# Performance work log

Measured on AMD Instinct MI355X. Metric: run time of the kernel, lower is better.

Reference implementation:

```python
import jax, jax.numpy as jnp
import numpy as np

N = 64
EPS = 1e-4
N_ITER = 100
BRANCH = 10


def setup_inputs() -> dict:
    key = jax.random.key(0)
    x = jax.random.normal(key, (8192, 4096), dtype=jnp.float32)
    return {"x": x}


def _lml(x):
    # x: [n_batch, nx], nx > N assumed (as configured in setup_inputs)
    n_batch, nx = x.shape
    x_sorted = jnp.sort(x, axis=1)[:, ::-1]  # descending
    nu_lower = -x_sorted[:, N - 1] - 7.0  # [n_batch]
    nu_upper = -x_sorted[:, N] + 7.0      # [n_batch]
    ls = jnp.linspace(0.0, 1.0, BRANCH).astype(x.dtype)  # [branch]
    rows = jnp.arange(n_batch)

    def cond(state):
        i, lo, hi = state
        return (i < N_ITER) & jnp.any(hi - lo > EPS)

    def body(state):
        i, lo, hi = state
        r = hi - lo                     # [n_batch]
        I = r > EPS                     # rows still being refined
        nus = r[:, None] * ls + lo[:, None]  # [n_batch, branch]
        # sigmoid-sum constraint at each candidate nu: [n_batch, branch]
        fs = jax.nn.sigmoid(x[:, None, :] + nus[:, :, None]).sum(axis=2) - N
        neg = (fs < 0).sum(axis=1) - 1  # index of last negative iterate
        J = neg < 0                     # all-positive-iterates warning case
        i_lower = jnp.clip(neg, 0, BRANCH - 2)
        new_lo = nus[rows, i_lower]
        new_hi = nus[rows, i_lower + 1]
        new_lo = jnp.where(J, new_lo - 7.0, new_lo)
        lo = jnp.where(I, new_lo, lo)
        hi = jnp.where(I, new_hi, hi)
        return i + 1, lo, hi

    _, lo, hi = jax.lax.while_loop(cond, body, (0, nu_lower, nu_upper))
    nu = lo + (hi - lo) / 2.0
    return jax.nn.sigmoid(x + nu[:, None])


def reference(x):
    return _lml(x)
```

## Files before the change

kernel.cpp:

```cpp
#include <hip/hip_runtime.h>

#define ROWLEN 4096
#define TPB    256
#define PER    16
#define NTARGET 64.0f
#define LOG2E  1.44269504088896340736f

__device__ __forceinline__ float exp2_fast(float x) {
    float r; asm("v_exp_f32 %0, %1" : "=v"(r) : "v"(x)); return r;
}
__device__ __forceinline__ float rcp_fast(float x) {
    float r; asm("v_rcp_f32 %0, %1" : "=v"(r) : "v"(x)); return r;
}
__device__ __forceinline__ float log2_fast(float x) {
    float r; asm("v_log_f32 %0, %1" : "=v"(r) : "v"(x)); return r;
}

__device__ __forceinline__ float sig_from(float v, float tnu) {
    float e = exp2_fast(fmaf(v, -LOG2E, tnu));
    return rcp_fast(1.0f + e);
}

__global__ __launch_bounds__(TPB) void lml_kernel(const float* __restrict__ x,
                                                  float* __restrict__ out) {
    const int t = threadIdx.x;
    const size_t base = (size_t)blockIdx.x * ROWLEN;

    float v[PER];
#pragma unroll
    for (int k = 0; k < 4; ++k) {
        float4 f = reinterpret_cast<const float4*>(x + base)[t + k * TPB];
        v[4*k+0] = f.x; v[4*k+1] = f.y; v[4*k+2] = f.z; v[4*k+3] = f.w;
    }

    float S = 0.0f, mn = v[0];
#pragma unroll
    for (int i = 0; i < PER; ++i) {
        S += exp2_fast(v[i] * LOG2E);
        mn = fminf(mn, v[i]);
    }

    __shared__ float lds[8];
    const int wave = t >> 6;
#pragma unroll
    for (int off = 32; off >= 1; off >>= 1) {
        S += __shfl_xor(S, off, 64);
        mn = fminf(mn, __shfl_xor(mn, off, 64));
    }
    if ((t & 63) == 0) { lds[wave] = S; lds[4 + wave] = mn; }
    __syncthreads();
    S  = (lds[0] + lds[1]) + (lds[2] + lds[3]);
    mn = fminf(fminf(lds[4], lds[5]), fminf(lds[6], lds[7]));
    __syncthreads();

    float nu = (6.0f - log2_fast(S)) * (1.0f / LOG2E);
    float lo = nu;
    float hi = -mn;

#pragma unroll 1
    for (int it = 0; it < 3; ++it) {
        const float tnu = -LOG2E * nu;
        float s = 0.0f, w = 0.0f;
#pragma unroll
        for (int i = 0; i < PER; ++i) {
            const float si = sig_from(v[i], tnu);
            s += si;
            w = fmaf(si, -si, w + si);
        }
#pragma unroll
        for (int off = 32; off >= 1; off >>= 1) {
            s += __shfl_xor(s, off, 64);
            w += __shfl_xor(w, off, 64);
        }
        if ((t & 63) == 0) { lds[wave] = s; lds[4 + wave] = w; }
        __syncthreads();
        const float fs = (lds[0] + lds[1]) + (lds[2] + lds[3]);
        const float fw = (lds[4] + lds[5]) + (lds[6] + lds[7]);
        __syncthreads();
        if (fs < NTARGET) lo = nu; else hi = nu;
        const float h = (log2_fast(fs) - 6.0f) * (1.0f / LOG2E);
        float nun = nu - h * fs * rcp_fast(fmaxf(fw, 1e-20f));
        if (!(nun > lo && nun < hi)) nun = 0.5f * (lo + hi);
        nu = nun;
    }

    const float tnu = -LOG2E * nu;
#pragma unroll
    for (int k = 0; k < 4; ++k) {
        float4 f;
        f.x = sig_from(v[4*k+0], tnu);
        f.y = sig_from(v[4*k+1], tnu);
        f.z = sig_from(v[4*k+2], tnu);
        f.w = sig_from(v[4*k+3], tnu);
        reinterpret_cast<float4*>(out + base)[t + k * TPB] = f;
    }
}

extern "C" void kernel_launch(void* const* d_in, const int* in_sizes, int n_in,
                              void* d_out, int out_size, void* d_ws, size_t ws_size,
                              hipStream_t stream) {
    const float* x = (const float*)d_in[0];
    float* out = (float*)d_out;
    const int rows = in_sizes[0] / ROWLEN;
    lml_kernel<<<rows, TPB, 0, stream>>>(x, out);
}
```

Baseline: 227.7 us.

## Map one row per wavefront, tighten initial bracket, drop a Newton iteration

Each 64-lane wavefront now owns a whole row and holds 64 values per lane, so reductions use only wave shuffles and need no LDS or block barriers. The initial upper bound is computed from a quadratic bound on the sums of exp and exp squared, and the midpoint seeds the solver. This allows Newton iterations to drop from three to two, and output uses nontemporal stores. The costs are higher register pressure and lower occupancy, plus the risk that two iterations lose accuracy on some rows.

After: 235.2 us. +3.3%, slower.

```diff
diff --git a/kernel.cpp b/kernel.cpp
--- a/kernel.cpp
+++ b/kernel.cpp
@@ -2,9 +2,9 @@
 
 #define ROWLEN 4096
 #define TPB    256
-#define PER    16
-#define NTARGET 64.0f
 #define LOG2E  1.44269504088896340736f
+
+typedef float f32x4 __attribute__((ext_vector_type(4)));
 
 __device__ __forceinline__ float exp2_fast(float x) {
     float r; asm("v_exp_f32 %0, %1" : "=v"(r) : "v"(x)); return r;
@@ -15,6 +15,9 @@
 __device__ __forceinline__ float log2_fast(float x) {
     float r; asm("v_log_f32 %0, %1" : "=v"(r) : "v"(x)); return r;
 }
+__device__ __forceinline__ float sqrt_fast(float x) {
+    float r; asm("v_sqrt_f32 %0, %1" : "=v"(r) : "v"(x)); return r;
+}
 
 __device__ __forceinline__ float sig_from(float v, float tnu) {
     float e = exp2_fast(fmaf(v, -LOG2E, tnu));
@@ -23,61 +26,66 @@
 
 __global__ __launch_bounds__(TPB) void lml_kernel(const float* __restrict__ x,
                                                   float* __restrict__ out) {
-    const int t = threadIdx.x;
-    const size_t base = (size_t)blockIdx.x * ROWLEN;
+    const int lane = threadIdx.x & 63;
+    const size_t row = (size_t)blockIdx.x * 4 + (threadIdx.x >> 6);
+    const f32x4* __restrict__ rp = reinterpret_cast<const f32x4*>(x + row * ROWLEN);
+    f32x4* __restrict__ op = reinterpret_cast<f32x4*>(out + row * ROWLEN);
 
-    float v[PER];
+    float v[64];
 #pragma unroll
-    for (int k = 0; k < 4; ++k) {
-        float4 f = reinterpret_cast<const float4*>(x + base)[t + k * TPB];
+    for (int k = 0; k < 16; ++k) {
+        f32x4 f = rp[k * 64 + lane];
         v[4*k+0] = f.x; v[4*k+1] = f.y; v[4*k+2] = f.z; v[4*k+3] = f.w;
     }
 
-    float S = 0.0f, mn = v[0];
+    float s10 = 0, s11 = 0, s12 = 0, s13 = 0;
+    float s20 = 0, s21 = 0, s22 = 0, s23 = 0;
 #pragma unroll
-    for (int i = 0; i < PER; ++i) {
-        S += exp2_fast(v[i] * LOG2E);
-        mn = fminf(mn, v[i]);
+    for (int k = 0; k < 16; ++k) {
+        float e0 = exp2_fast(v[4*k+0] * LOG2E);
+        float e1 = exp2_fast(v[4*k+1] * LOG2E);
+        float e2 = exp2_fast(v[4*k+2] * LOG2E);
+        float e3 = exp2_fast(v[4*k+3] * LOG2E);
+        s10 += e0; s11 += e1; s12 += e2; s13 += e3;
+        s20 = fmaf(e0, e0, s20); s21 = fmaf(e1, e1, s21);
+        s22 = fmaf(e2, e2, s22); s23 = fmaf(e3, e3, s23);
+    }
+    float S1 = (s10 + s11) + (s12 + s13);
+    float S2 = (s20 + s21) + (s22 + s23);
+#pragma unroll
+    for (int off = 32; off >= 1; off >>= 1) {
+        S1 += __shfl_xor(S1, off, 64);
+        S2 += __shfl_xor(S2, off, 64);
     }
 
-    __shared__ float lds[8];
-    const int wave = t >> 6;
-#pragma unroll
-    for (int off = 32; off >= 1; off >>= 1) {
-        S += __shfl_xor(S, off, 64);
-        mn = fminf(mn, __shfl_xor(mn, off, 64));
-    }
-    if ((t & 63) == 0) { lds[wave] = S; lds[4 + wave] = mn; }
-    __syncthreads();
-    S  = (lds[0] + lds[1]) + (lds[2] + lds[3]);
-    mn = fminf(fminf(lds[4], lds[5]), fminf(lds[6], lds[7]));
-    __syncthreads();
-
-    float nu = (6.0f - log2_fast(S)) * (1.0f / LOG2E);
-    float lo = nu;
-    float hi = -mn;
+    float disc = fmaxf(fmaf(S1, S1, -256.0f * S2), 0.0f);
+    float lo = (6.0f - log2_fast(S1)) * (1.0f / LOG2E);
+    float hi = (7.0f - log2_fast(S1 + sqrt_fast(disc))) * (1.0f / LOG2E);
+    float nu = 0.5f * (lo + hi);
 
 #pragma unroll 1
-    for (int it = 0; it < 3; ++it) {
+    for (int it = 0; it < 2; ++it) {
         const float tnu = -LOG2E * nu;
-        float s = 0.0f, w = 0.0f;
+        float a0 = 0, a1 = 0, a2 = 0, a3 = 0;
+        float b0 = 0, b1 = 0, b2 = 0, b3 = 0;
 #pragma unroll
-        for (int i = 0; i < PER; ++i) {
-            const float si = sig_from(v[i], tnu);
-            s += si;
-            w = fmaf(si, -si, w + si);
+        for (int k = 0; k < 16; ++k) {
+            float x0 = sig_from(v[4*k+0], tnu);
+            float x1 = sig_from(v[4*k+1], tnu);
+            float x2 = sig_from(v[4*k+2], tnu);
+            float x3 = sig_from(v[4*k+3], tnu);
+            a0 += x0; a1 += x1; a2 += x2; a3 += x3;
+            b0 = fmaf(x0, -x0, b0 + x0); b1 = fmaf(x1, -x1, b1 + x1);
+            b2 = fmaf(x2, -x2, b2 + x2); b3 = fmaf(x3, -x3, b3 + x3);
         }
+        float fs = (a0 + a1) + (a2 + a3);
+        float fw = (b0 + b1) + (b2 + b3);
 #pragma unroll
         for (int off = 32; off >= 1; off >>= 1) {
-            s += __shfl_xor(s, off, 64);
-            w += __shfl_xor(w, off, 64);
+            fs += __shfl_xor(fs, off, 64);
+            fw += __shfl_xor(fw, off, 64);
         }
-        if ((t & 63) == 0) { lds[wave] = s; lds[4 + wave] = w; }
-        __syncthreads();
-        const float fs = (lds[0] + lds[1]) + (lds[2] + lds[3]);
-        const float fw = (lds[4] + lds[5]) + (lds[6] + lds[7]);
-        __syncthreads();
-        if (fs < NTARGET) lo = nu; else hi = nu;
+        if (fs < 64.0f) lo = nu; else hi = nu;
         const float h = (log2_fast(fs) - 6.0f) * (1.0f / LOG2E);
         float nun = nu - h * fs * rcp_fast(fmaxf(fw, 1e-20f));
         if (!(nun > lo && nun < hi)) nun = 0.5f * (lo + hi);
@@ -86,13 +94,13 @@
 
     const float tnu = -LOG2E * nu;
 #pragma unroll
-    for (int k = 0; k < 4; ++k) {
-        float4 f;
+    for (int k = 0; k < 16; ++k) {
+        f32x4 f;
         f.x = sig_from(v[4*k+0], tnu);
         f.y = sig_from(v[4*k+1], tnu);
         f.z = sig_from(v[4*k+2], tnu);
         f.w = sig_from(v[4*k+3], tnu);
-        reinterpret_cast<float4*>(out + base)[t + k * TPB] = f;
+        __builtin_nontemporal_store(f, op + k * 64 + lane);
     }
 }
 
@@ -102,5 +110,5 @@
     const float* x = (const float*)d_in[0];
     float* out = (float*)d_out;
     const int rows = in_sizes[0] / ROWLEN;
-    lml_kernel<<<rows, TPB, 0, stream>>>(x, out);
+    lml_kernel<<<rows / 4, TPB, 0, stream>>>(x, out);
 }
```
